# Kernel tuning notes

Measured on AMD Instinct MI355X. Metric: run time of the kernel, lower is better.

## Reference

```python
import jax, jax.numpy as jnp
import numpy as np

N_NODES = 50000
N_EDGES = 800000
IN_F, EDGE_F, HID, HEADS, OUT_F = 128, 16, 32, 4, 128
NEG_SLOPE = 0.2


def edge_gat_layer(h, ef, src, dst, W, We, al, ar, ae, b, act):
    """One DGL-style EdgeGATConv layer.
    h: [N, Fin], ef: [E, Fe], W: [Fin, H*D], We: [Fe, H*D],
    al/ar/ae: [H, D], b: [H*D]. Returns [N, H*D].
    """
    N = h.shape[0]
    H, D = al.shape
    feat = (h @ W).reshape(N, H, D)                    # [N,H,D]
    fe = (ef @ We).reshape(-1, H, D)                   # [E,H,D]
    el = jnp.einsum('nhd,hd->nh', feat, al)            # [N,H]
    er = jnp.einsum('nhd,hd->nh', feat, ar)            # [N,H]
    ee = jnp.einsum('ehd,hd->eh', fe, ae)              # [E,H]
    e = jax.nn.leaky_relu(el[src] + er[dst] + ee, NEG_SLOPE)  # [E,H]
    # edge softmax over incoming edges of each dst node
    emax = jax.ops.segment_max(e, dst, num_segments=N)        # [N,H]
    ex = jnp.exp(e - emax[dst])                               # [E,H]
    esum = jax.ops.segment_sum(ex, dst, num_segments=N)       # [N,H]
    a = ex / esum[dst]                                        # [E,H]
    msg = feat[src] * a[:, :, None]                           # [E,H,D]
    rst = jax.ops.segment_sum(msg, dst, num_segments=N)       # [N,H,D]
    rst = rst + b.reshape(1, H, D)
    if act:
        rst = jax.nn.relu(rst)
    return rst.reshape(N, H * D)


def _glorot(k, shape):
    fan = shape[0]
    return jax.random.normal(k, shape, dtype=jnp.float32) / np.sqrt(fan)


def setup_inputs() -> dict:
    key = jax.random.key(0)
    ks = jax.random.split(key, 24)
    inp = {
        'h': jax.random.normal(ks[0], (N_NODES, IN_F), dtype=jnp.float32),
        'edge_feats': jax.random.normal(ks[1], (N_EDGES, EDGE_F), dtype=jnp.float32),
        'src': jax.random.randint(ks[2], (N_EDGES,), 0, N_NODES, dtype=jnp.int32),
        'dst': jax.random.randint(ks[3], (N_EDGES,), 0, N_NODES, dtype=jnp.int32),
    }
    # layer 0: IN_F -> HEADS*HID ; layer 1: HEADS*HID -> HEADS*HID ; layer 2: heads=1, OUT_F
    dims = [(IN_F, HEADS, HID), (HEADS * HID, HEADS, HID), (HEADS * HID, 1, OUT_F)]
    ki = 4
    for i, (fin, H, D) in enumerate(dims):
        inp[f'W{i}'] = _glorot(ks[ki], (fin, H * D)); ki += 1
        inp[f'We{i}'] = _glorot(ks[ki], (EDGE_F, H * D)); ki += 1
        inp[f'al{i}'] = _glorot(ks[ki], (H, D)); ki += 1
        inp[f'ar{i}'] = _glorot(ks[ki], (H, D)); ki += 1
        inp[f'ae{i}'] = _glorot(ks[ki], (H, D)); ki += 1
        inp[f'b{i}'] = jnp.zeros((H * D,), dtype=jnp.float32)
    return inp


def reference(h, edge_feats, src, dst,
              W0, We0, al0, ar0, ae0, b0,
              W1, We1, al1, ar1, ae1, b1,
              W2, We2, al2, ar2, ae2, b2):
    h = edge_gat_layer(h, edge_feats, src, dst, W0, We0, al0, ar0, ae0, b0, True)
    h = edge_gat_layer(h, edge_feats, src, dst, W1, We1, al1, ar1, ae1, b1, True)
    h = edge_gat_layer(h, edge_feats, src, dst, W2, We2, al2, ar2, ae2, b2, False)
    return h
```

## Files before the change

kernel.cpp:

```cpp
#include <hip/hip_runtime.h>
#include <hip/hip_fp16.h>
#include <cstdint>

#define NN 50000
#define NE 800000
static constexpr int HD = 128;
static constexpr int EF_DIM = 16;
static constexpr int SCAN_B = 256;
static constexpr int NPARTS = (NN + SCAN_B - 1) / SCAN_B;

typedef _Float16 f16x4 __attribute__((ext_vector_type(4)));
typedef float f32x4 __attribute__((ext_vector_type(4)));


__global__ void k_hist(const int* __restrict__ dst, int* __restrict__ deg) {
    int e = blockIdx.x * blockDim.x + threadIdx.x;
    if (e < NE) atomicAdd(&deg[dst[e]], 1);
}

__global__ __launch_bounds__(SCAN_B) void k_part(const int* __restrict__ deg,
                                                 int* __restrict__ part) {
    __shared__ int s[SCAN_B];
    int t = threadIdx.x;
    int i = blockIdx.x * SCAN_B + t;
    s[t] = (i < NN) ? deg[i] : 0;
    __syncthreads();
    for (int off = SCAN_B / 2; off > 0; off >>= 1) {
        if (t < off) s[t] += s[t + off];
        __syncthreads();
    }
    if (t == 0) part[blockIdx.x] = s[0];
}

__global__ __launch_bounds__(SCAN_B) void k_scanpart(int* __restrict__ part) {
    __shared__ int s[SCAN_B];
    int t = threadIdx.x;
    int v = (t < NPARTS) ? part[t] : 0;
    s[t] = v;
    __syncthreads();
    for (int off = 1; off < SCAN_B; off <<= 1) {
        int u = (t >= off) ? s[t - off] : 0;
        __syncthreads();
        s[t] += u;
        __syncthreads();
    }
    if (t < NPARTS) part[t] = s[t] - v;
}

__global__ __launch_bounds__(SCAN_B) void k_rowptr(const int* __restrict__ deg,
                                                   const int* __restrict__ part,
                                                   int* __restrict__ row_ptr,
                                                   int* __restrict__ cursor) {
    __shared__ int s[SCAN_B];
    int t = threadIdx.x;
    int i = blockIdx.x * SCAN_B + t;
    int v = (i < NN) ? deg[i] : 0;
    s[t] = v;
    __syncthreads();
    for (int off = 1; off < SCAN_B; off <<= 1) {
        int u = (t >= off) ? s[t - off] : 0;
        __syncthreads();
        s[t] += u;
        __syncthreads();
    }
    int excl = s[t] - v + part[blockIdx.x];
    if (i < NN) { row_ptr[i] = excl; cursor[i] = excl; }
    if (i == NN) row_ptr[NN] = NE;
}

__global__ void k_scatter(const int* __restrict__ src, const int* __restrict__ dst,
                          int* __restrict__ cursor, int2* __restrict__ epr) {
    int e = blockIdx.x * blockDim.x + threadIdx.x;
    if (e >= NE) return;
    int d = dst[e];
    int pos = atomicAdd(&cursor[d], 1);
    epr[pos] = make_int2(e, src[e]);
}

__global__ __launch_bounds__(256) void k_segsort(const int* __restrict__ row_ptr,
                                                 const int2* __restrict__ epr,
                                                 int* __restrict__ ssrc,
                                                 int* __restrict__ eidx) {
    __shared__ int2 seg[4][128];
    const int wave = threadIdx.x >> 6;
    const int lane = threadIdx.x & 63;
    const int n = blockIdx.x * 4 + wave;
    const int start = row_ptr[n];
    const int len = row_ptr[n + 1] - start;
    const bool small = (len > 0 && len <= 128);
    if (small)
        for (int s = lane; s < len; s += 64) seg[wave][s] = epr[start + s];
    __syncthreads();
    if (small) {
        for (int s = lane; s < len; s += 64) {
            int2 me = seg[wave][s];
            int rank = 0;
            for (int j = 0; j < len; j++) {
                int2 o = seg[wave][j];
                rank += (o.y < me.y) || (o.y == me.y && o.x < me.x);
            }
            ssrc[start + rank] = me.y;
            eidx[start + rank] = me.x;
        }
    } else if (len > 128) {
        for (int s = lane; s < len; s += 64) {
            int2 v = epr[start + s];
            ssrc[start + s] = v.y;
            eidx[start + s] = v.x;
        }
    }
}

__global__ void k_M3(const float* __restrict__ We0, const float* __restrict__ ae0,
                     const float* __restrict__ We1, const float* __restrict__ ae1,
                     const float* __restrict__ We2, const float* __restrict__ ae2,
                     float* __restrict__ M) {
    int l = blockIdx.x;
    int t = threadIdx.x;
    const float* We = (l == 0) ? We0 : (l == 1) ? We1 : We2;
    const float* ae = (l == 0) ? ae0 : (l == 1) ? ae1 : ae2;
    int H = (l == 2) ? 1 : 4;
    int D = (l == 2) ? 128 : 32;
    if (t >= EF_DIM * H) return;
    int f = t / H, h = t % H;
    float s = 0.f;
    for (int d = 0; d < D; d++) s += We[f * HD + h * D + d] * ae[h * D + d];
    M[l * 64 + f * H + h] = s;
}

__global__ __launch_bounds__(256) void k_eproj(const float* __restrict__ EFt,
                                               const int* __restrict__ eidx,
                                               const float* __restrict__ M,
                                               float4* __restrict__ ep0,
                                               float4* __restrict__ ep1,
                                               float* __restrict__ ep2) {
    __shared__ float sM[192];
    int t = threadIdx.x;
    if (t < 192) sM[t] = M[t];
    __syncthreads();
    int i = blockIdx.x * 256 + t;
    if (i >= NE) return;
    int e = eidx[i];
    float ef[EF_DIM];
    const float4* efp = (const float4*)(EFt + (size_t)e * EF_DIM);
#pragma unroll
    for (int q = 0; q < 4; q++) {
        float4 v = efp[q];
        ef[4 * q] = v.x; ef[4 * q + 1] = v.y; ef[4 * q + 2] = v.z; ef[4 * q + 3] = v.w;
    }
    float o0[4] = {0.f, 0.f, 0.f, 0.f};
    float o1[4] = {0.f, 0.f, 0.f, 0.f};
    float o2 = 0.f;
#pragma unroll
    for (int f = 0; f < EF_DIM; f++) {
        float v = ef[f];
#pragma unroll
        for (int h = 0; h < 4; h++) {
            o0[h] += v * sM[f * 4 + h];
            o1[h] += v * sM[64 + f * 4 + h];
        }
        o2 += v * sM[128 + f];
    }
    ep0[i] = make_float4(o0[0], o0[1], o0[2], o0[3]);
    ep1[i] = make_float4(o1[0], o1[1], o1[2], o1[3]);
    ep2[i] = o2;
}

__global__ void k_cvt(const float* __restrict__ in, _Float16* __restrict__ out, int n4) {
    int i = blockIdx.x * blockDim.x + threadIdx.x;
    if (i >= n4) return;
    float4 v = ((const float4*)in)[i];
    f16x4 o = {(_Float16)v.x, (_Float16)v.y, (_Float16)v.z, (_Float16)v.w};
    ((f16x4*)out)[i] = o;
}


__global__ __launch_bounds__(256) void k_feat(const _Float16* __restrict__ Xh,
                                              const float* __restrict__ W,
                                              _Float16* __restrict__ Fh) {
    __shared__ _Float16 Wt[128][136];
    const int t = threadIdx.x;
    const int lane = t & 63;
    const int wv = t >> 6;
    for (int i = t; i < 128 * 128; i += 256) {
        int k = i >> 7, nn = i & 127;
        Wt[nn][k] = (_Float16)W[i];
    }
    const int nbase = blockIdx.x * 64;
    const int row = nbase + wv * 16 + (lane & 15);
    const int rclamp = (row < NN) ? row : NN - 1;
    const int ksub = (lane >> 4) * 4;
    f16x4 a[8];
#pragma unroll
    for (int kb = 0; kb < 8; kb++)
        a[kb] = *(const f16x4*)(Xh + (size_t)rclamp * 128 + kb * 16 + ksub);
    __syncthreads();
#pragma unroll
    for (int nt = 0; nt < 8; nt++) {
        f32x4 acc = {0.f, 0.f, 0.f, 0.f};
        const int nc = nt * 16 + (lane & 15);
#pragma unroll
        for (int kb = 0; kb < 8; kb++) {
            f16x4 bf = *(const f16x4*)(&Wt[nc][kb * 16 + ksub]);
            acc = __builtin_amdgcn_mfma_f32_16x16x16f16(a[kb], bf, acc, 0, 0, 0);
        }
        const int r0 = nbase + wv * 16 + (lane >> 4) * 4;
#pragma unroll
        for (int r = 0; r < 4; r++) {
            int ro = r0 + r;
            if (ro < NN) Fh[(size_t)ro * 128 + nt * 16 + (lane & 15)] = (_Float16)acc[r];
        }
    }
}

__global__ void k_elr(const __half2* __restrict__ Fh, const float* __restrict__ al,
                      const float* __restrict__ ar, float* __restrict__ el,
                      float* __restrict__ er, int H, int D) {
    int idx = blockIdx.x * blockDim.x + threadIdx.x;
    if (idx >= NN * H) return;
    int n = idx / H, h = idx % H;
    const __half2* fr = Fh + (size_t)n * 64 + h * (D / 2);
    const float2* alr = (const float2*)(al + h * D);
    const float2* arr = (const float2*)(ar + h * D);
    float sl = 0.f, sr = 0.f;
    for (int q = 0; q < D / 2; q++) {
        float2 v = __half22float2(fr[q]);
        float2 A = alr[q], B = arr[q];
        sl += v.x * A.x + v.y * A.y;
        sr += v.x * B.x + v.y * B.y;
    }
    el[idx] = sl;
    er[idx] = sr;
}

__global__ __launch_bounds__(256) void k_node(const int* __restrict__ row_ptr,
                                              const int* __restrict__ ssrc,
                                              const float* __restrict__ ep,
                                              const float* __restrict__ el,
                                              const float* __restrict__ er,
                                              const __half2* __restrict__ Fh,
                                              const float* __restrict__ bias,
                                              float* __restrict__ Rf,
                                              _Float16* __restrict__ Rh,
                                              int H, int D, int act, int out16) {
    __shared__ float wlds[4][256];
    const int wave = threadIdx.x >> 6;
    const int lane = threadIdx.x & 63;
    const int n = blockIdx.x * 4 + wave;
    const int start = row_ptr[n];
    const int end = row_ptr[n + 1];
    const int len = end - start;
    const int slots = len * H;
    const int c = 2 * lane;
    const int hcol = c / D;
    float2 b2 = make_float2(bias[c], bias[c + 1]);
    float2 a = make_float2(0.f, 0.f);

    if (len > 0) {
        const int hsh = (H == 4) ? 2 : 0;
        const int hh = lane & (H - 1);
        const float er_j = er[n * H + hh];
        const float* epb = ep + (size_t)start * H;
        float pmax = -3.0e38f, psum = 0.f;

        if (slots <= 256) {
            float* wp = wlds[wave];
            for (int jj = lane; jj < slots; jj += 64) {
                int i = start + (jj >> hsh);
                float x = el[ssrc[i] * H + hh] + er_j + epb[jj];
                x = (x > 0.f) ? x : 0.2f * x;
                wp[jj] = x;
                pmax = fmaxf(pmax, x);
            }
            for (int m = H; m < 64; m <<= 1) pmax = fmaxf(pmax, __shfl_xor(pmax, m));
            for (int jj = lane; jj < slots; jj += 64) {
                float ex = __expf(wp[jj] - pmax);
                wp[jj] = ex;
                psum += ex;
            }
            for (int m = H; m < 64; m <<= 1) psum += __shfl_xor(psum, m);
            const float inv = 1.f / __shfl(psum, hcol);
#pragma unroll 4
            for (int i = start; i < end; i++) {
                float w = wp[(i - start) * H + hcol];
                float2 f2 = __half22float2(Fh[(size_t)ssrc[i] * 64 + lane]);
                a.x += f2.x * w;
                a.y += f2.y * w;
            }
            a.x *= inv;
            a.y *= inv;
        } else {
            for (int jj = lane; jj < slots; jj += 64) {
                int i = start + (jj >> hsh);
                float x = el[ssrc[i] * H + hh] + er_j + epb[jj];
                x = (x > 0.f) ? x : 0.2f * x;
                pmax = fmaxf(pmax, x);
            }
            for (int m = H; m < 64; m <<= 1) pmax = fmaxf(pmax, __shfl_xor(pmax, m));
            for (int jj = lane; jj < slots; jj += 64) {
                int i = start + (jj >> hsh);
                float x = el[ssrc[i] * H + hh] + er_j + epb[jj];
                x = (x > 0.f) ? x : 0.2f * x;
                psum += __expf(x - pmax);
            }
            for (int m = H; m < 64; m <<= 1) psum += __shfl_xor(psum, m);
            const float inv = 1.f / __shfl(psum, hcol);
            const float pm_c = __shfl(pmax, hcol);
            const float er_c = er[n * H + hcol];
            for (int i = start; i < end; i++) {
                int sn = ssrc[i];
                float x = el[sn * H + hcol] + er_c + epb[(i - start) * H + hcol];
                x = (x > 0.f) ? x : 0.2f * x;
                float w = __expf(x - pm_c);
                float2 f2 = __half22float2(Fh[(size_t)sn * 64 + lane]);
                a.x += f2.x * w;
                a.y += f2.y * w;
            }
            a.x *= inv;
            a.y *= inv;
        }
    }

    float2 v = make_float2(a.x + b2.x, a.y + b2.y);
    if (act) { v.x = fmaxf(v.x, 0.f); v.y = fmaxf(v.y, 0.f); }
    if (out16)
        ((__half2*)Rh)[(size_t)n * 64 + lane] = __floats2half2_rn(v.x, v.y);
    else
        ((float2*)Rf)[(size_t)n * 64 + lane] = v;
}


static void run_layer(const _Float16* Xh, const int* ssrc, const int* row_ptr,
                      const float* W, const float* al, const float* ar,
                      const float* b, const float* ep, int H, int D, int act,
                      _Float16* Fh, float* el, float* er,
                      float* Rf, _Float16* Rh, int out16, hipStream_t stream) {
    const int NH = NN * H;
    hipLaunchKernelGGL(k_feat, dim3((NN + 63) / 64), dim3(256), 0, stream, Xh, W, Fh);
    hipLaunchKernelGGL(k_elr, dim3((NH + 255) / 256), dim3(256), 0, stream,
                       (const __half2*)Fh, al, ar, el, er, H, D);
    hipLaunchKernelGGL(k_node, dim3(NN / 4), dim3(256), 0, stream,
                       row_ptr, ssrc, ep, el, er, (const __half2*)Fh, b,
                       Rf, Rh, H, D, act, out16);
}

extern "C" void kernel_launch(void* const* d_in, const int* in_sizes, int n_in,
                              void* d_out, int out_size, void* d_ws, size_t ws_size,
                              hipStream_t stream) {
    const float* h   = (const float*)d_in[0];
    const float* eft = (const float*)d_in[1];
    const int* src   = (const int*)d_in[2];
    const int* dst   = (const int*)d_in[3];
    auto P = [&](int i) { return (const float*)d_in[i]; };

    float* ws = (float*)d_ws;
    _Float16* Fh   = (_Float16*)ws;
    _Float16* Xh   = (_Float16*)(ws + (size_t)3200000);
    float* ep0     = ws + (size_t)6400000;
    float* ep1     = ep0 + (size_t)NE * 4;
    float* ep2     = ep1 + (size_t)NE * 4;
    float* el      = ep2 + (size_t)NE;
    float* er      = el + (size_t)NN * 4;
    float* M       = er + (size_t)NN * 4;
    int2* epr      = (int2*)(M + 192);
    int* ssrc      = (int*)(epr + NE);
    int* eidx      = ssrc + NE;
    int* row_ptr   = eidx + NE;
    int* cursor    = row_ptr + (NN + 1);
    int* deg       = cursor + NN;
    int* part      = deg + NN;
    float* out     = (float*)d_out;

    hipMemsetAsync(deg, 0, NN * sizeof(int), stream);
    hipLaunchKernelGGL(k_hist, dim3((NE + 255) / 256), dim3(256), 0, stream, dst, deg);
    hipLaunchKernelGGL(k_part, dim3(NPARTS), dim3(SCAN_B), 0, stream, deg, part);
    hipLaunchKernelGGL(k_scanpart, dim3(1), dim3(SCAN_B), 0, stream, part);
    hipLaunchKernelGGL(k_rowptr, dim3(NPARTS), dim3(SCAN_B), 0, stream,
                       deg, part, row_ptr, cursor);
    hipLaunchKernelGGL(k_scatter, dim3((NE + 255) / 256), dim3(256), 0, stream,
                       src, dst, cursor, epr);
    hipLaunchKernelGGL(k_segsort, dim3(NN / 4), dim3(256), 0, stream,
                       row_ptr, epr, ssrc, eidx);
    hipLaunchKernelGGL(k_M3, dim3(3), dim3(64), 0, stream,
                       P(5), P(8), P(11), P(14), P(17), P(20), M);
    hipLaunchKernelGGL(k_eproj, dim3((NE + 255) / 256), dim3(256), 0, stream,
                       eft, eidx, M, (float4*)ep0, (float4*)ep1, ep2);
    hipLaunchKernelGGL(k_cvt, dim3((NN * 128 / 4 + 255) / 256), dim3(256), 0, stream,
                       h, Xh, NN * 128 / 4);

    run_layer(Xh, ssrc, row_ptr, P(4), P(6), P(7), P(9), ep0,
              4, 32, 1, Fh, el, er, nullptr, Xh, 1, stream);
    run_layer(Xh, ssrc, row_ptr, P(10), P(12), P(13), P(15), ep1,
              4, 32, 1, Fh, el, er, nullptr, Xh, 1, stream);
    run_layer(Xh, ssrc, row_ptr, P(16), P(18), P(19), P(21), ep2,
              1, 128, 0, Fh, el, er, out, nullptr, 0, stream);
}
```

Measured before the change: 411.8 us.

## Fuse attention-logit computation into projection GEMM and merge setup kernels

Folds the el/er dot products into k_feat's MFMA epilogue using shuffle reductions, which removes the separate k_elr pass over Fh. The weight transpose to fp16 is precomputed once in a combined prep kernel that also zeroes deg, builds M and converts h, replacing a memset and several tiny launches. Segsort now sorts epr in place instead of splitting into ssrc/eidx arrays. Edge projections are stored as fp16 to halve their traffic, and k_node is templated on H/D/out16. Costs are extra register pressure in k_feat, fp16 rounding of edge logits, and wider int2 reads in k_node.

```diff
diff --git a/kernel.cpp b/kernel.cpp
--- a/kernel.cpp
+++ b/kernel.cpp
@@ -11,6 +11,51 @@
 
 typedef _Float16 f16x4 __attribute__((ext_vector_type(4)));
 typedef float f32x4 __attribute__((ext_vector_type(4)));
+
+__global__ __launch_bounds__(256) void k_prep(const float* __restrict__ h,
+        const float* __restrict__ We0, const float* __restrict__ ae0,
+        const float* __restrict__ We1, const float* __restrict__ ae1,
+        const float* __restrict__ We2, const float* __restrict__ ae2,
+        const float* __restrict__ W0, const float* __restrict__ W1,
+        const float* __restrict__ W2,
+        int* __restrict__ deg, float* __restrict__ M,
+        _Float16* __restrict__ Wht, _Float16* __restrict__ Xh) {
+    const int b = blockIdx.x, t = threadIdx.x;
+    if (b < 196) {
+        int i = b * 256 + t;
+        if (i < NN) deg[i] = 0;
+        return;
+    }
+    if (b < 199) {
+        int l = b - 196;
+        const float* We = (l == 0) ? We0 : (l == 1) ? We1 : We2;
+        const float* ae = (l == 0) ? ae0 : (l == 1) ? ae1 : ae2;
+        int H = (l == 2) ? 1 : 4, D = (l == 2) ? 128 : 32;
+        if (t < EF_DIM * H) {
+            int f = t / H, hh = t % H;
+            float s = 0.f;
+            for (int d = 0; d < D; d++) s += We[f * HD + hh * D + d] * ae[hh * D + d];
+            M[l * 64 + f * H + hh] = s;
+        }
+        return;
+    }
+    if (b < 391) {
+        int i = (b - 199) * 256 + t;
+        int l = i >> 14, rem = i & 16383;
+        int n = rem >> 7, k = rem & 127;
+        const float* W = (l == 0) ? W0 : (l == 1) ? W1 : W2;
+        Wht[(size_t)l * 16384 + n * 128 + k] = (_Float16)W[k * 128 + n];
+        return;
+    }
+    {
+        int i = (b - 391) * 256 + t;
+        if (i < NN * 32) {
+            float4 v = ((const float4*)h)[i];
+            f16x4 o = {(_Float16)v.x, (_Float16)v.y, (_Float16)v.z, (_Float16)v.w};
+            ((f16x4*)Xh)[i] = o;
+        }
+    }
+}
 
 
 __global__ void k_hist(const int* __restrict__ dst, int* __restrict__ deg) {
@@ -78,9 +123,7 @@
 }
 
 __global__ __launch_bounds__(256) void k_segsort(const int* __restrict__ row_ptr,
-                                                 const int2* __restrict__ epr,
-                                                 int* __restrict__ ssrc,
-                                                 int* __restrict__ eidx) {
+                                                 int2* __restrict__ epr) {
     __shared__ int2 seg[4][128];
     const int wave = threadIdx.x >> 6;
     const int lane = threadIdx.x & 63;
@@ -99,48 +142,24 @@
                 int2 o = seg[wave][j];
                 rank += (o.y < me.y) || (o.y == me.y && o.x < me.x);
             }
-            ssrc[start + rank] = me.y;
-            eidx[start + rank] = me.x;
-        }
-    } else if (len > 128) {
-        for (int s = lane; s < len; s += 64) {
-            int2 v = epr[start + s];
-            ssrc[start + s] = v.y;
-            eidx[start + s] = v.x;
-        }
-    }
-}
-
-__global__ void k_M3(const float* __restrict__ We0, const float* __restrict__ ae0,
-                     const float* __restrict__ We1, const float* __restrict__ ae1,
-                     const float* __restrict__ We2, const float* __restrict__ ae2,
-                     float* __restrict__ M) {
-    int l = blockIdx.x;
-    int t = threadIdx.x;
-    const float* We = (l == 0) ? We0 : (l == 1) ? We1 : We2;
-    const float* ae = (l == 0) ? ae0 : (l == 1) ? ae1 : ae2;
-    int H = (l == 2) ? 1 : 4;
-    int D = (l == 2) ? 128 : 32;
-    if (t >= EF_DIM * H) return;
-    int f = t / H, h = t % H;
-    float s = 0.f;
-    for (int d = 0; d < D; d++) s += We[f * HD + h * D + d] * ae[h * D + d];
-    M[l * 64 + f * H + h] = s;
+            epr[start + rank] = me;
+        }
+    }
 }
 
 __global__ __launch_bounds__(256) void k_eproj(const float* __restrict__ EFt,
-                                               const int* __restrict__ eidx,
+                                               const int2* __restrict__ epr,
                                                const float* __restrict__ M,
-                                               float4* __restrict__ ep0,
-                                               float4* __restrict__ ep1,
-                                               float* __restrict__ ep2) {
+                                               _Float16* __restrict__ ep0,
+                                               _Float16* __restrict__ ep1,
+                                               _Float16* __restrict__ ep2) {
     __shared__ float sM[192];
     int t = threadIdx.x;
     if (t < 192) sM[t] = M[t];
     __syncthreads();
     int i = blockIdx.x * 256 + t;
     if (i >= NE) return;
-    int e = eidx[i];
+    int e = epr[i].x;
     float ef[EF_DIM];
     const float4* efp = (const float4*)(EFt + (size_t)e * EF_DIM);
 #pragma unroll
@@ -155,94 +174,114 @@
     for (int f = 0; f < EF_DIM; f++) {
         float v = ef[f];
 #pragma unroll
-        for (int h = 0; h < 4; h++) {
-            o0[h] += v * sM[f * 4 + h];
-            o1[h] += v * sM[64 + f * 4 + h];
+        for (int hh = 0; hh < 4; hh++) {
+            o0[hh] += v * sM[f * 4 + hh];
+            o1[hh] += v * sM[64 + f * 4 + hh];
         }
         o2 += v * sM[128 + f];
     }
-    ep0[i] = make_float4(o0[0], o0[1], o0[2], o0[3]);
-    ep1[i] = make_float4(o1[0], o1[1], o1[2], o1[3]);
-    ep2[i] = o2;
-}
-
-__global__ void k_cvt(const float* __restrict__ in, _Float16* __restrict__ out, int n4) {
-    int i = blockIdx.x * blockDim.x + threadIdx.x;
-    if (i >= n4) return;
-    float4 v = ((const float4*)in)[i];
-    f16x4 o = {(_Float16)v.x, (_Float16)v.y, (_Float16)v.z, (_Float16)v.w};
-    ((f16x4*)out)[i] = o;
-}
-
-
+    f16x4 a = {(_Float16)o0[0], (_Float16)o0[1], (_Float16)o0[2], (_Float16)o0[3]};
+    f16x4 c = {(_Float16)o1[0], (_Float16)o1[1], (_Float16)o1[2], (_Float16)o1[3]};
+    ((f16x4*)ep0)[i] = a;
+    ((f16x4*)ep1)[i] = c;
+    ep2[i] = (_Float16)o2;
+}
+
+
+template <int H>
 __global__ __launch_bounds__(256) void k_feat(const _Float16* __restrict__ Xh,
-                                              const float* __restrict__ W,
-                                              _Float16* __restrict__ Fh) {
-    __shared__ _Float16 Wt[128][136];
+                                              const _Float16* __restrict__ Wht,
+                                              const float* __restrict__ al,
+                                              const float* __restrict__ ar,
+                                              _Float16* __restrict__ Fh,
+                                              float* __restrict__ el,
+                                              float* __restrict__ er) {
     const int t = threadIdx.x;
     const int lane = t & 63;
     const int wv = t >> 6;
-    for (int i = t; i < 128 * 128; i += 256) {
-        int k = i >> 7, nn = i & 127;
-        Wt[nn][k] = (_Float16)W[i];
-    }
+    const int l15 = lane & 15;
+    const int kg = lane >> 4;
     const int nbase = blockIdx.x * 64;
-    const int row = nbase + wv * 16 + (lane & 15);
-    const int rclamp = (row < NN) ? row : NN - 1;
-    const int ksub = (lane >> 4) * 4;
+    const int arow = nbase + wv * 16 + l15;
+    const int rclamp = (arow < NN) ? arow : NN - 1;
+    const int ksub = kg * 4;
     f16x4 a[8];
 #pragma unroll
     for (int kb = 0; kb < 8; kb++)
         a[kb] = *(const f16x4*)(Xh + (size_t)rclamp * 128 + kb * 16 + ksub);
-    __syncthreads();
+
+    const int r0 = nbase + wv * 16 + kg * 4;
+    float slp[4][H], srp[4][H];
+#pragma unroll
+    for (int r = 0; r < 4; r++)
+#pragma unroll
+        for (int hh = 0; hh < H; hh++) { slp[r][hh] = 0.f; srp[r][hh] = 0.f; }
+
 #pragma unroll
     for (int nt = 0; nt < 8; nt++) {
         f32x4 acc = {0.f, 0.f, 0.f, 0.f};
-        const int nc = nt * 16 + (lane & 15);
+        const int nc = nt * 16 + l15;
+        const _Float16* wp = Wht + (size_t)nc * 128;
 #pragma unroll
         for (int kb = 0; kb < 8; kb++) {
-            f16x4 bf = *(const f16x4*)(&Wt[nc][kb * 16 + ksub]);
+            f16x4 bf = *(const f16x4*)(wp + kb * 16 + ksub);
             acc = __builtin_amdgcn_mfma_f32_16x16x16f16(a[kb], bf, acc, 0, 0, 0);
         }
-        const int r0 = nbase + wv * 16 + (lane >> 4) * 4;
+        const float alv = al[nc], arv = ar[nc];
+        constexpr int HSEL = 0;
+        const int hsel = (H == 4) ? (nt >> 1) : HSEL;
 #pragma unroll
         for (int r = 0; r < 4; r++) {
             int ro = r0 + r;
-            if (ro < NN) Fh[(size_t)ro * 128 + nt * 16 + (lane & 15)] = (_Float16)acc[r];
-        }
-    }
-}
-
-__global__ void k_elr(const __half2* __restrict__ Fh, const float* __restrict__ al,
-                      const float* __restrict__ ar, float* __restrict__ el,
-                      float* __restrict__ er, int H, int D) {
-    int idx = blockIdx.x * blockDim.x + threadIdx.x;
-    if (idx >= NN * H) return;
-    int n = idx / H, h = idx % H;
-    const __half2* fr = Fh + (size_t)n * 64 + h * (D / 2);
-    const float2* alr = (const float2*)(al + h * D);
-    const float2* arr = (const float2*)(ar + h * D);
-    float sl = 0.f, sr = 0.f;
-    for (int q = 0; q < D / 2; q++) {
-        float2 v = __half22float2(fr[q]);
-        float2 A = alr[q], B = arr[q];
-        sl += v.x * A.x + v.y * A.y;
-        sr += v.x * B.x + v.y * B.y;
-    }
-    el[idx] = sl;
-    er[idx] = sr;
-}
-
+            if (ro < NN) Fh[(size_t)ro * 128 + nc] = (_Float16)acc[r];
+            slp[r][hsel] += acc[r] * alv;
+            srp[r][hsel] += acc[r] * arv;
+        }
+    }
+
+#pragma unroll
+    for (int m = 1; m < 16; m <<= 1)
+#pragma unroll
+        for (int r = 0; r < 4; r++)
+#pragma unroll
+            for (int hh = 0; hh < H; hh++) {
+                slp[r][hh] += __shfl_xor(slp[r][hh], m);
+                srp[r][hh] += __shfl_xor(srp[r][hh], m);
+            }
+
+    if (H == 4) {
+        int r = l15 >> 2, hh2 = l15 & 3;
+        float sv = 0.f, ev = 0.f;
+#pragma unroll
+        for (int rr = 0; rr < 4; rr++)
+#pragma unroll
+            for (int hc = 0; hc < H; hc++)
+                if (rr == r && hc == hh2) { sv = slp[rr][hc]; ev = srp[rr][hc]; }
+        int ro = r0 + r;
+        if (ro < NN) { el[ro * 4 + hh2] = sv; er[ro * 4 + hh2] = ev; }
+    } else {
+        if (l15 < 4) {
+            float sv = 0.f, ev = 0.f;
+#pragma unroll
+            for (int rr = 0; rr < 4; rr++)
+                if (rr == l15) { sv = slp[rr][0]; ev = srp[rr][0]; }
+            int ro = r0 + l15;
+            if (ro < NN) { el[ro] = sv; er[ro] = ev; }
+        }
+    }
+}
+
+template <int H, int D, int OUT16>
 __global__ __launch_bounds__(256) void k_node(const int* __restrict__ row_ptr,
-                                              const int* __restrict__ ssrc,
-                                              const float* __restrict__ ep,
+                                              const int2* __restrict__ epr,
+                                              const _Float16* __restrict__ ep,
                                               const float* __restrict__ el,
                                               const float* __restrict__ er,
                                               const __half2* __restrict__ Fh,
                                               const float* __restrict__ bias,
                                               float* __restrict__ Rf,
                                               _Float16* __restrict__ Rh,
-                                              int H, int D, int act, int out16) {
+                                              int act) {
     __shared__ float wlds[4][256];
     const int wave = threadIdx.x >> 6;
     const int lane = threadIdx.x & 63;
@@ -257,17 +296,17 @@
     float2 a = make_float2(0.f, 0.f);
 
     if (len > 0) {
-        const int hsh = (H == 4) ? 2 : 0;
+        constexpr int hsh = (H == 4) ? 2 : 0;
         const int hh = lane & (H - 1);
         const float er_j = er[n * H + hh];
-        const float* epb = ep + (size_t)start * H;
+        const _Float16* epb = ep + (size_t)start * H;
         float pmax = -3.0e38f, psum = 0.f;
 
         if (slots <= 256) {
             float* wp = wlds[wave];
             for (int jj = lane; jj < slots; jj += 64) {
                 int i = start + (jj >> hsh);
-                float x = el[ssrc[i] * H + hh] + er_j + epb[jj];
+                float x = el[epr[i].y * H + hh] + er_j + (float)epb[jj];
                 x = (x > 0.f) ? x : 0.2f * x;
                 wp[jj] = x;
                 pmax = fmaxf(pmax, x);
@@ -283,7 +322,7 @@
 #pragma unroll 4
             for (int i = start; i < end; i++) {
                 float w = wp[(i - start) * H + hcol];
-                float2 f2 = __half22float2(Fh[(size_t)ssrc[i] * 64 + lane]);
+                float2 f2 = __half22float2(Fh[(size_t)epr[i].y * 64 + lane]);
                 a.x += f2.x * w;
                 a.y += f2.y * w;
             }
@@ -292,14 +331,14 @@
         } else {
             for (int jj = lane; jj < slots; jj += 64) {
                 int i = start + (jj >> hsh);
-                float x = el[ssrc[i] * H + hh] + er_j + epb[jj];
+                float x = el[epr[i].y * H + hh] + er_j + (float)epb[jj];
                 x = (x > 0.f) ? x : 0.2f * x;
                 pmax = fmaxf(pmax, x);
             }
             for (int m = H; m < 64; m <<= 1) pmax = fmaxf(pmax, __shfl_xor(pmax, m));
             for (int jj = lane; jj < slots; jj += 64) {
                 int i = start + (jj >> hsh);
-                float x = el[ssrc[i] * H + hh] + er_j + epb[jj];
+                float x = el[epr[i].y * H + hh] + er_j + (float)epb[jj];
                 x = (x > 0.f) ? x : 0.2f * x;
                 psum += __expf(x - pmax);
             }
@@ -308,8 +347,8 @@
             const float pm_c = __shfl(pmax, hcol);
             const float er_c = er[n * H + hcol];
             for (int i = start; i < end; i++) {
-                int sn = ssrc[i];
-                float x = el[sn * H + hcol] + er_c + epb[(i - start) * H + hcol];
+                int sn = epr[i].y;
+                float x = el[sn * H + hcol] + er_c + (float)epb[(i - start) * H + hcol];
                 x = (x > 0.f) ? x : 0.2f * x;
                 float w = __expf(x - pm_c);
                 float2 f2 = __half22float2(Fh[(size_t)sn * 64 + lane]);
@@ -323,26 +362,12 @@
 
     float2 v = make_float2(a.x + b2.x, a.y + b2.y);
     if (act) { v.x = fmaxf(v.x, 0.f); v.y = fmaxf(v.y, 0.f); }
-    if (out16)
+    if (OUT16)
         ((__half2*)Rh)[(size_t)n * 64 + lane] = __floats2half2_rn(v.x, v.y);
     else
         ((float2*)Rf)[(size_t)n * 64 + lane] = v;
 }
 
-
-static void run_layer(const _Float16* Xh, const int* ssrc, const int* row_ptr,
-                      const float* W, const float* al, const float* ar,
-                      const float* b, const float* ep, int H, int D, int act,
-                      _Float16* Fh, float* el, float* er,
-                      float* Rf, _Float16* Rh, int out16, hipStream_t stream) {
-    const int NH = NN * H;
-    hipLaunchKernelGGL(k_feat, dim3((NN + 63) / 64), dim3(256), 0, stream, Xh, W, Fh);
-    hipLaunchKernelGGL(k_elr, dim3((NH + 255) / 256), dim3(256), 0, stream,
-                       (const __half2*)Fh, al, ar, el, er, H, D);
-    hipLaunchKernelGGL(k_node, dim3(NN / 4), dim3(256), 0, stream,
-                       row_ptr, ssrc, ep, el, er, (const __half2*)Fh, b,
-                       Rf, Rh, H, D, act, out16);
-}
 
 extern "C" void kernel_launch(void* const* d_in, const int* in_sizes, int n_in,
                               void* d_out, int out_size, void* d_ws, size_t ws_size,
@@ -355,23 +380,24 @@
 
     float* ws = (float*)d_ws;
     _Float16* Fh   = (_Float16*)ws;
-    _Float16* Xh   = (_Float16*)(ws + (size_t)3200000);
-    float* ep0     = ws + (size_t)6400000;
-    float* ep1     = ep0 + (size_t)NE * 4;
-    float* ep2     = ep1 + (size_t)NE * 4;
-    float* el      = ep2 + (size_t)NE;
+    _Float16* Xh   = Fh + (size_t)NN * 128;
+    _Float16* Wht  = Xh + (size_t)NN * 128;
+    _Float16* ep0  = Wht + 3 * 16384;
+    _Float16* ep1  = ep0 + (size_t)NE * 4;
+    _Float16* ep2  = ep1 + (size_t)NE * 4;
+    float* el      = (float*)(ep2 + NE);
     float* er      = el + (size_t)NN * 4;
     float* M       = er + (size_t)NN * 4;
     int2* epr      = (int2*)(M + 192);
-    int* ssrc      = (int*)(epr + NE);
-    int* eidx      = ssrc + NE;
-    int* row_ptr   = eidx + NE;
+    int* row_ptr   = (int*)(epr + NE);
     int* cursor    = row_ptr + (NN + 1);
     int* deg       = cursor + NN;
     int* part      = deg + NN;
     float* out     = (float*)d_out;
 
-    hipMemsetAsync(deg, 0, NN * sizeof(int), stream);
+    hipLaunchKernelGGL(k_prep, dim3(391 + (NN * 32 + 255) / 256), dim3(256), 0, stream,
+                       h, P(5), P(8), P(11), P(14), P(17), P(20),
+                       P(4), P(10), P(16), deg, M, Wht, Xh);
     hipLaunchKernelGGL(k_hist, dim3((NE + 255) / 256), dim3(256), 0, stream, dst, deg);
     hipLaunchKernelGGL(k_part, dim3(NPARTS), dim3(SCAN_B), 0, stream, deg, part);
     hipLaunchKernelGGL(k_scanpart, dim3(1), dim3(SCAN_B), 0, stream, part);
@@ -379,19 +405,24 @@
                        deg, part, row_ptr, cursor);
     hipLaunchKernelGGL(k_scatter, dim3((NE + 255) / 256), dim3(256), 0, stream,
                        src, dst, cursor, epr);
-    hipLaunchKernelGGL(k_segsort, dim3(NN / 4), dim3(256), 0, stream,
-                       row_ptr, epr, ssrc, eidx);
-    hipLaunchKernelGGL(k_M3, dim3(3), dim3(64), 0, stream,
-                       P(5), P(8), P(11), P(14), P(17), P(20), M);
+    hipLaunchKernelGGL(k_segsort, dim3(NN / 4), dim3(256), 0, stream, row_ptr, epr);
     hipLaunchKernelGGL(k_eproj, dim3((NE + 255) / 256), dim3(256), 0, stream,
-                       eft, eidx, M, (float4*)ep0, (float4*)ep1, ep2);
-    hipLaunchKernelGGL(k_cvt, dim3((NN * 128 / 4 + 255) / 256), dim3(256), 0, stream,
-                       h, Xh, NN * 128 / 4);
-
-    run_layer(Xh, ssrc, row_ptr, P(4), P(6), P(7), P(9), ep0,
-              4, 32, 1, Fh, el, er, nullptr, Xh, 1, stream);
-    run_layer(Xh, ssrc, row_ptr, P(10), P(12), P(13), P(15), ep1,
-              4, 32, 1, Fh, el, er, nullptr, Xh, 1, stream);
-    run_layer(Xh, ssrc, row_ptr, P(16), P(18), P(19), P(21), ep2,
-              1, 128, 0, Fh, el, er, out, nullptr, 0, stream);
-}
+                       eft, epr, M, ep0, ep1, ep2);
+
+    const int FG = (NN + 63) / 64;
+    hipLaunchKernelGGL((k_feat<4>), dim3(FG), dim3(256), 0, stream,
+                       Xh, Wht, P(6), P(7), Fh, el, er);
+    hipLaunchKernelGGL((k_node<4, 32, 1>), dim3(NN / 4), dim3(256), 0, stream,
+                       row_ptr, epr, ep0, el, er, (const __half2*)Fh, P(9),
+                       nullptr, Xh, 1);
+    hipLaunchKernelGGL((k_feat<4>), dim3(FG), dim3(256), 0, stream,
+                       Xh, Wht + 16384, P(12), P(13), Fh, el, er);
+    hipLaunchKernelGGL((k_node<4, 32, 1>), dim3(NN / 4), dim3(256), 0, stream,
+                       row_ptr, epr, ep1, el, er, (const __half2*)Fh, P(15),
+                       nullptr, Xh, 1);
+    hipLaunchKernelGGL((k_feat<1>), dim3(FG), dim3(256), 0, stream,
+                       Xh, Wht + 32768, P(18), P(19), Fh, el, er);
+    hipLaunchKernelGGL((k_node<1, 128, 0>), dim3(NN / 4), dim3(256), 0, stream,
+                       row_ptr, epr, ep2, el, er, (const __half2*)Fh, P(21),
+                       out, nullptr, 0);
+}
```

New measurement: 411.1 us. About the same (-0.2%).
